# Kernel tuning notes

Measured on AMD Instinct MI355X. Metric: run time of the kernel, lower is better.

The kernel has to match this reference:

```python
import jax, jax.numpy as jnp
import numpy as np

KS = (7, 7)
ST = (3, 3)
PD = (3, 3)
DIM = 512
HID = 1960  # 40 * 49, divisible by kernel_shape


def _patch_flat_idx(out_h, out_w):
    kh, kw = KS; sh, sw = ST; ph, pw = PD
    oh = (out_h + 2 * ph - kh) // sh + 1
    ow = (out_w + 2 * pw - kw) // sw + 1
    Wp = out_w + 2 * pw
    iy = jnp.arange(kh)[:, None, None, None] + (jnp.arange(oh) * sh)[None, None, :, None]
    ix = jnp.arange(kw)[None, :, None, None] + (jnp.arange(ow) * sw)[None, None, None, :]
    # (kh, kw, oh, ow) flat index into padded image
    return (iy * Wp + ix), oh, ow


def fold(patches, out_h, out_w):
    # patches: (B, C*kh*kw, L) -> (B, C, out_h, out_w), overlap-add like F.fold
    kh, kw = KS; ph, pw = PD
    idx, oh, ow = _patch_flat_idx(out_h, out_w)
    B, CK, L = patches.shape
    C = CK // (kh * kw)
    Hp, Wp = out_h + 2 * ph, out_w + 2 * pw
    p = patches.reshape(B, C, kh, kw, oh, ow)
    out = jnp.zeros((B, C, Hp * Wp), patches.dtype)
    out = out.at[:, :, idx.reshape(-1)].add(p.reshape(B, C, -1))
    return out.reshape(B, C, Hp, Wp)[:, :, ph:ph + out_h, pw:pw + out_w]


def unfold(img, out_h, out_w):
    # img: (B, C, H, W) -> (B, C*kh*kw, L), like F.unfold
    kh, kw = KS; ph, pw = PD
    idx, oh, ow = _patch_flat_idx(out_h, out_w)
    B, C = img.shape[:2]
    imgp = jnp.pad(img, ((0, 0), (0, 0), (ph, ph), (pw, pw)))
    flat = imgp.reshape(B, C, -1)
    g = flat[:, :, idx.reshape(-1)].reshape(B, C, kh, kw, oh, ow)
    return g.reshape(B, C * kh * kw, oh * ow)


def setup_inputs() -> dict:
    key = jax.random.key(0)
    k1, k2, k3, k4, k5 = jax.random.split(key, 5)
    x = jax.random.normal(k1, (2, 5760, DIM), dtype=jnp.float32)
    W1 = jax.random.normal(k2, (HID, DIM), dtype=jnp.float32) * 0.02
    b1 = jax.random.normal(k3, (HID,), dtype=jnp.float32) * 0.02
    W2 = jax.random.normal(k4, (DIM, HID), dtype=jnp.float32) * 0.02
    b2 = jax.random.normal(k5, (DIM,), dtype=jnp.float32) * 0.02
    return {"x": x, "W1": W1, "b1": b1, "W2": W2, "b2": b2, "out_h": 60, "out_w": 108}


def reference(x, W1, b1, W2, b2, out_h, out_w):
    kh, kw = KS; sh, sw = ST; ph, pw = PD
    oh = (out_h + 2 * ph - kh) // sh + 1
    ow = (out_w + 2 * pw - kw) // sw + 1
    n_vecs = oh * ow
    h = jnp.einsum('bnd,hd->bnh', x, W1) + b1          # (b, n, HID)
    b_, n, c = h.shape
    p = h.reshape(-1, n_vecs, c).transpose(0, 2, 1)     # (B', c, L)
    folded = fold(p, out_h, out_w)                      # (B', c//49, H, W)
    ones = jnp.ones((p.shape[0], kh * kw, n_vecs), h.dtype)
    norm = fold(ones, out_h, out_w)                     # (B', 1, H, W)
    y = unfold(folded / norm, out_h, out_w)             # (B', c, L)
    y = y.transpose(0, 2, 1).reshape(b_, n, c)
    out = jnp.einsum('bnh,dh->bnd', jax.nn.gelu(y, approximate=False), W2) + b2
    return out
```

## Files before the change

### kernel.cpp

```cpp
#include <hip/hip_runtime.h>
#include <cmath>

#define M_ROWS   11520
#define DIM      512
#define HID      1960
#define HIDP     2048
#define KP2      1984
#define OH       20
#define OW       36
#define LVEC     720
#define NCH      40
#define BPRIME   16
#define HP       66
#define WP       114

typedef unsigned short u16;
typedef __bf16 bf16x8 __attribute__((ext_vector_type(8)));
typedef float  f32x4  __attribute__((ext_vector_type(4)));

__device__ __forceinline__ u16 f2bf(float f) {
    unsigned u = __float_as_uint(f);
    u += 0x7fffu + ((u >> 16) & 1u);
    return (u16)(u >> 16);
}
__device__ __forceinline__ float bf2f(u16 h) {
    return __uint_as_float(((unsigned)h) << 16);
}

__device__ __forceinline__ void gload_lds16(const void* g, void* l) {
    __builtin_amdgcn_global_load_lds(
        (const __attribute__((address_space(1))) void*)g,
        (__attribute__((address_space(3))) void*)l, 16, 0, 0);
}
__device__ __forceinline__ void gload_lds4(const void* g, void* l) {
    __builtin_amdgcn_global_load_lds(
        (const __attribute__((address_space(1))) void*)g,
        (__attribute__((address_space(3))) void*)l, 4, 0, 0);
}

#define CVT_XB   5760
#define CVT_W1B  1024
#define CVT_W2B  1024
#define CVT_Z    270
__global__ __launch_bounds__(256) void cvt_all(const float* __restrict__ x,
                                               const float* __restrict__ W1,
                                               const float* __restrict__ W2,
                                               u16* __restrict__ xb,
                                               u16* __restrict__ W1b,
                                               u16* __restrict__ W2b,
                                               u16* __restrict__ g2) {
    const int b = blockIdx.x;
    const int tid = threadIdx.x;
    ushort4 o;
    if (b < CVT_XB) {
        int i = (b * 256 + tid) * 4;
        float4 v = *(const float4*)(x + i);
        o.x = f2bf(v.x); o.y = f2bf(v.y); o.z = f2bf(v.z); o.w = f2bf(v.w);
        *(ushort4*)(xb + i) = o;
    } else if (b < CVT_XB + CVT_W1B) {
        int i = ((b - CVT_XB) * 256 + tid) * 4;
        if (i < HID * DIM) {
            float4 v = *(const float4*)(W1 + i);
            o.x = f2bf(v.x); o.y = f2bf(v.y); o.z = f2bf(v.z); o.w = f2bf(v.w);
        } else {
            o.x = o.y = o.z = o.w = 0;
        }
        *(ushort4*)(W1b + i) = o;
    } else if (b < CVT_XB + CVT_W1B + CVT_W2B) {
        int i = ((b - CVT_XB - CVT_W1B) * 256 + tid) * 4;
        int d = i / HIDP, c = i - d * HIDP;
        if (c < HID) {
            float4 v = *(const float4*)(W2 + (size_t)d * HID + c);
            o.x = f2bf(v.x); o.y = f2bf(v.y); o.z = f2bf(v.z); o.w = f2bf(v.w);
        } else {
            o.x = o.y = o.z = o.w = 0;
        }
        *(ushort4*)(W2b + i) = o;
    } else {
        int i = ((b - CVT_XB - CVT_W1B - CVT_W2B) * 256 + tid) * 4;
        int row = i / 24, c = i - row * 24;
        o.x = o.y = o.z = o.w = 0;
        *(ushort4*)(g2 + (size_t)row * HIDP + HID + c) = o;
    }
}

template <int OUT_BF16, int BN>
__global__ __launch_bounds__(512) void gemm_bt(const u16* __restrict__ A,
                                               const u16* __restrict__ B,
                                               const float* __restrict__ bias,
                                               int biasN, void* __restrict__ Cout,
                                               int N, int K, int ldk) {
    constexpr int WN = BN / 2;
    constexpr int NU = WN / 16;
    constexpr int BCH = BN * 8;

    __shared__ u16 sA[128 * 64];
    __shared__ u16 sB[BN * 64];

    const int tid  = threadIdx.x;
    const int ntn  = N / BN;
    const int NB   = gridDim.x;
    const int v    = (blockIdx.x & 7) * (NB >> 3) + (blockIdx.x >> 3);
    const int bm   = v / ntn;
    const int bn   = v - bm * ntn;
    const int lane = tid & 63;
    const int wv   = tid >> 6;
    const int wm   = (wv >> 1) * 32;
    const int wn   = (wv & 1) * WN;
    const int r    = lane & 15;
    const int quad = lane >> 4;

    const size_t Arow0 = (size_t)bm * 128 * ldk;
    const size_t Brow0 = (size_t)bn * BN * ldk;

    f32x4 acc[2][NU] = {};

    for (int kt = 0; kt < K; kt += 64) {
        __syncthreads();
#pragma unroll
        for (int i = 0; i < 2; i++) {
            int e   = i * 512 + tid;
            int row = e >> 3;
            int cp  = e & 7;
            int cg  = cp ^ (row & 7);
            gload_lds16(A + Arow0 + (size_t)row * ldk + kt + cg * 8, (char*)sA + e * 16);
        }
#pragma unroll
        for (int i = 0; i < BCH / 512; i++) {
            int e   = i * 512 + tid;
            int row = e >> 3;
            int cp  = e & 7;
            int cg  = cp ^ (row & 7);
            gload_lds16(B + Brow0 + (size_t)row * ldk + kt + cg * 8, (char*)sB + e * 16);
        }
        __syncthreads();
#pragma unroll
        for (int kk = 0; kk < 2; kk++) {
            bf16x8 af[2], bg[NU];
#pragma unroll
            for (int t = 0; t < 2; t++) {
                int row = wm + t * 16 + r;
                int c   = (kk * 4 + quad) ^ (row & 7);
                af[t] = *(const bf16x8*)(sA + row * 64 + c * 8);
            }
#pragma unroll
            for (int u = 0; u < NU; u++) {
                int row = wn + u * 16 + r;
                int c   = (kk * 4 + quad) ^ (row & 7);
                bg[u] = *(const bf16x8*)(sB + row * 64 + c * 8);
            }
#pragma unroll
            for (int t = 0; t < 2; t++)
#pragma unroll
                for (int u = 0; u < NU; u++)
                    acc[t][u] = __builtin_amdgcn_mfma_f32_16x16x32_bf16(
                        af[t], bg[u], acc[t][u], 0, 0, 0);
        }
    }

    const int gm0 = bm * 128 + wm;
    const int gn0 = bn * BN + wn;
#pragma unroll
    for (int u = 0; u < NU; u++) {
        int gn = gn0 + u * 16 + r;
        float bv = (gn < biasN) ? bias[gn] : 0.0f;
#pragma unroll
        for (int t = 0; t < 2; t++) {
            int gm = gm0 + t * 16 + quad * 4;
#pragma unroll
            for (int q = 0; q < 4; q++) {
                float v2 = acc[t][u][q] + bv;
                if (OUT_BF16)
                    ((u16*)Cout)[(size_t)(gm + q) * N + gn] = f2bf(v2);
                else
                    ((float*)Cout)[(size_t)(gm + q) * N + gn] = v2;
            }
        }
    }
}

__global__ __launch_bounds__(512) void mid_fused(const u16* __restrict__ hg,
                                                 u16* __restrict__ g2) {
    __shared__ u16 sh[12 * OW * 50];
    __shared__ u16 sG[34 * WP];
    __shared__ u16 rowoff[10 * OW];
    __shared__ u16 kidx[49];

    const int b  = blockIdx.x;
    const int bp = b / (NCH * 2);
    const int rr = b - bp * (NCH * 2);
    const int ch = rr >> 1;
    const int s  = rr & 1;
    const int o0 = s * 10;
    const int lo = s * 8;
    const int n0 = bp * LVEC;
    const int c0 = ch * 49;
    const int c0e = c0 & ~1;
    const int koff = c0 - c0e;
    const int tid = threadIdx.x;

    if (tid < 10 * OW) {
        int oy = tid / OW, ox = tid - oy * OW;
        rowoff[tid] = (u16)(342 * oy + 3 * ox);
    } else if (tid < 10 * OW + 49) {
        int k = tid - 10 * OW;
        int ky = k / 7;
        kidx[k] = (u16)(114 * ky + (k - 7 * ky));
    }

    {
        const char* hb = (const char*)(hg + (size_t)(n0 + lo * OW) * HIDP + c0e);
        for (int i = tid; i < 12 * OW * 25; i += 512) {
            int l = i / 25, j = i - l * 25;
            gload_lds4(hb + (size_t)l * (HIDP * 2) + j * 4, (char*)sh + i * 4);
        }
    }
    __syncthreads();

    const int px = tid & 127;
    const int rg = tid >> 7;
    if (px < WP) {
        const bool pxin = (px >= 3) && (px <= 110);
        const int kx0 = px % 3;
        int  ct[3];
        bool vx[3];
        int  cx = 0;
#pragma unroll
        for (int dx = 0; dx < 3; dx++) {
            int kx = kx0 + 3 * dx, rx = px - kx;
            bool ok = pxin && (kx <= 6) && (rx >= 0) && (rx <= 105);
            vx[dx] = ok;
            ct[dx] = ok ? ((rx / 3) * 50 + kx) : 0;
            cx += ok ? 1 : 0;
        }
        const float fcx = (cx == 3) ? (1.0f / 3.0f) : ((cx == 2) ? 0.5f : 1.0f);

        for (int pr = rg; pr < 34; pr += 4) {
            int py = 3 * o0 + pr;
            float val = 0.0f;
            if (pxin && py >= 3 && py <= 62) {
                int ky0 = py % 3;
                float sum = 0.0f;
                int cy = 0;
#pragma unroll
                for (int dy = 0; dy < 3; dy++) {
                    int ky = ky0 + 3 * dy, ry = py - ky;
                    if (ky <= 6 && ry >= 0 && ry <= 57) {
                        int rt = (ry / 3 - lo) * (OW * 50) + ky * 7 + koff;
                        cy++;
                        float v0 = bf2f(sh[rt + ct[0]]);
                        float v1 = bf2f(sh[rt + ct[1]]);
                        float v2 = bf2f(sh[rt + ct[2]]);
                        sum += vx[0] ? v0 : 0.0f;
                        sum += vx[1] ? v1 : 0.0f;
                        sum += vx[2] ? v2 : 0.0f;
                    }
                }
                float fcy = (cy == 3) ? (1.0f / 3.0f) : ((cy == 2) ? 0.5f : 1.0f);
                float m = sum * fcx * fcy;
                val = 0.5f * m * (1.0f + erff(m * 0.70710678118654752f));
            }
            sG[pr * WP + px] = f2bf(val);
        }
    }
    __syncthreads();

    {
        u16* g2row = g2 + (size_t)(n0 + o0 * OW) * HIDP + c0;
        int l = tid / 49;
        int k = tid - l * 49;
        int soff = l * HIDP + k;
        for (int i = tid; i < 10 * OW * 49; i += 512) {
            g2row[soff] = sG[rowoff[l] + kidx[k]];
            l += 10; k += 22; soff += 10 * HIDP + 22;
            if (k >= 49) { k -= 49; l += 1; soff += HIDP - 49; }
        }
    }
}

extern "C" void kernel_launch(void* const* d_in, const int* in_sizes, int n_in,
                              void* d_out, int out_size, void* d_ws, size_t ws_size,
                              hipStream_t stream) {
    (void)in_sizes; (void)n_in; (void)out_size; (void)ws_size;
    const float* x  = (const float*)d_in[0];
    const float* W1 = (const float*)d_in[1];
    const float* b1 = (const float*)d_in[2];
    const float* W2 = (const float*)d_in[3];
    const float* b2 = (const float*)d_in[4];
    float* out = (float*)d_out;

    char* ws = (char*)d_ws;
    u16* xb  = (u16*)(ws);
    u16* W1b = (u16*)(ws + 11796480);
    u16* W2b = (u16*)(ws + 13893632);
    u16* hg  = (u16*)(ws + 15990784);
    u16* g2  = (u16*)(ws + 63176704);

    cvt_all<<<CVT_XB + CVT_W1B + CVT_W2B + CVT_Z, 256, 0, stream>>>(
        x, W1, W2, xb, W1b, W2b, g2);

    gemm_bt<1, 128><<<(M_ROWS / 128) * (HIDP / 128), 512, 0, stream>>>(
        xb, W1b, b1, HID, (void*)hg, HIDP, DIM, DIM);

    mid_fused<<<BPRIME * NCH * 2, 512, 0, stream>>>(hg, g2);

    gemm_bt<0, 64><<<(M_ROWS / 128) * (DIM / 64), 512, 0, stream>>>(
        g2, W2b, b2, DIM, (void*)out, DIM, KP2, HIDP);
}
```

Baseline: 188.3 us.

## Split mid_fused tiles horizontally and load patches with 16-byte LDS transfers

The fold/normalize/gelu/unfold kernel now splits each tile into two horizontal halves, doubling the grid to 2560 blocks with a smaller shared-memory footprint. The patch load switches from 4-byte to 16-byte global-to-LDS transfers on 8-element-aligned channel windows, with index math done by multiply-shift division. The aim is better occupancy and fewer, wider memory transactions, at the cost of halo columns loaded twice and extra index arithmetic in the write-back loop.

```diff
diff --git a/kernel.cpp b/kernel.cpp
--- a/kernel.cpp
+++ b/kernel.cpp
@@ -31,11 +31,6 @@
     __builtin_amdgcn_global_load_lds(
         (const __attribute__((address_space(1))) void*)g,
         (__attribute__((address_space(3))) void*)l, 16, 0, 0);
-}
-__device__ __forceinline__ void gload_lds4(const void* g, void* l) {
-    __builtin_amdgcn_global_load_lds(
-        (const __attribute__((address_space(1))) void*)g,
-        (__attribute__((address_space(3))) void*)l, 4, 0, 0);
 }
 
 #define CVT_XB   5760
@@ -181,61 +176,57 @@
 
 __global__ __launch_bounds__(512) void mid_fused(const u16* __restrict__ hg,
                                                  u16* __restrict__ g2) {
-    __shared__ u16 sh[12 * OW * 50];
-    __shared__ u16 sG[34 * WP];
-    __shared__ u16 rowoff[10 * OW];
-    __shared__ u16 kidx[49];
-
-    const int b  = blockIdx.x;
-    const int bp = b / (NCH * 2);
-    const int rr = b - bp * (NCH * 2);
-    const int ch = rr >> 1;
-    const int s  = rr & 1;
-    const int o0 = s * 10;
-    const int lo = s * 8;
-    const int n0 = bp * LVEC;
-    const int c0 = ch * 49;
-    const int c0e = c0 & ~1;
-    const int koff = c0 - c0e;
+    __shared__ u16 sh[12 * 20 * 56];
+    __shared__ u16 sG[34 * 58];
+
+    const int b   = blockIdx.x;
+    const int bp  = b / (NCH * 4);
+    const int rr  = b - bp * (NCH * 4);
+    const int ch  = rr >> 2;
+    const int s   = (rr >> 1) & 1;
+    const int xh  = rr & 1;
+    const int o0  = s * 10;
+    const int lo  = s * 8;
+    const int ox0 = xh * 16;
+    const int n0  = bp * LVEC;
+    const int c0  = ch * 49;
+    const int c0f = c0 & ~7;
+    const int koff = c0 & 7;
     const int tid = threadIdx.x;
 
-    if (tid < 10 * OW) {
-        int oy = tid / OW, ox = tid - oy * OW;
-        rowoff[tid] = (u16)(342 * oy + 3 * ox);
-    } else if (tid < 10 * OW + 49) {
-        int k = tid - 10 * OW;
-        int ky = k / 7;
-        kidx[k] = (u16)(114 * ky + (k - 7 * ky));
-    }
-
     {
-        const char* hb = (const char*)(hg + (size_t)(n0 + lo * OW) * HIDP + c0e);
-        for (int i = tid; i < 12 * OW * 25; i += 512) {
-            int l = i / 25, j = i - l * 25;
-            gload_lds4(hb + (size_t)l * (HIDP * 2) + j * 4, (char*)sh + i * 4);
+        const char* hb = (const char*)(hg + (size_t)(n0 + lo * 36 + ox0) * HIDP + c0f);
+        for (int t = tid; t < 12 * 20 * 7; t += 512) {
+            int r   = (int)(((unsigned)t * 74899u) >> 19);
+            int c   = t - r * 7;
+            int loy = (int)(((unsigned)r * 3277u) >> 16);
+            int oxl = r - 20 * loy;
+            gload_lds16(hb + (size_t)(loy * 36 + oxl) * (HIDP * 2) + c * 16,
+                        (char*)sh + t * 16);
         }
     }
     __syncthreads();
 
-    const int px = tid & 127;
-    const int rg = tid >> 7;
-    if (px < WP) {
-        const bool pxin = (px >= 3) && (px <= 110);
-        const int kx0 = px % 3;
+    const int pxl = tid & 63;
+    const int rg  = tid >> 6;
+    if (pxl < 58) {
+        const int  pxg  = pxl + 54 * xh;
+        const bool pxin = (pxg >= 3) && (pxg <= 110);
+        const int  kx0  = pxg % 3;
         int  ct[3];
         bool vx[3];
         int  cx = 0;
 #pragma unroll
         for (int dx = 0; dx < 3; dx++) {
-            int kx = kx0 + 3 * dx, rx = px - kx;
+            int kx = kx0 + 3 * dx, rx = pxg - kx;
             bool ok = pxin && (kx <= 6) && (rx >= 0) && (rx <= 105);
             vx[dx] = ok;
-            ct[dx] = ok ? ((rx / 3) * 50 + kx) : 0;
+            ct[dx] = ok ? ((rx / 3) - ox0) * 56 + kx : 0;
             cx += ok ? 1 : 0;
         }
         const float fcx = (cx == 3) ? (1.0f / 3.0f) : ((cx == 2) ? 0.5f : 1.0f);
 
-        for (int pr = rg; pr < 34; pr += 4) {
+        for (int pr = rg; pr < 34; pr += 8) {
             int py = 3 * o0 + pr;
             float val = 0.0f;
             if (pxin && py >= 3 && py <= 62) {
@@ -246,7 +237,7 @@
                 for (int dy = 0; dy < 3; dy++) {
                     int ky = ky0 + 3 * dy, ry = py - ky;
                     if (ky <= 6 && ry >= 0 && ry <= 57) {
-                        int rt = (ry / 3 - lo) * (OW * 50) + ky * 7 + koff;
+                        int rt = (ry / 3 - lo) * (20 * 56) + ky * 7 + koff;
                         cy++;
                         float v0 = bf2f(sh[rt + ct[0]]);
                         float v1 = bf2f(sh[rt + ct[1]]);
@@ -260,20 +251,22 @@
                 float m = sum * fcx * fcy;
                 val = 0.5f * m * (1.0f + erff(m * 0.70710678118654752f));
             }
-            sG[pr * WP + px] = f2bf(val);
+            sG[pr * 58 + pxl] = f2bf(val);
         }
     }
     __syncthreads();
 
     {
-        u16* g2row = g2 + (size_t)(n0 + o0 * OW) * HIDP + c0;
-        int l = tid / 49;
-        int k = tid - l * 49;
-        int soff = l * HIDP + k;
-        for (int i = tid; i < 10 * OW * 49; i += 512) {
-            g2row[soff] = sG[rowoff[l] + kidx[k]];
-            l += 10; k += 22; soff += 10 * HIDP + 22;
-            if (k >= 49) { k -= 49; l += 1; soff += HIDP - 49; }
+        u16* g2row = g2 + (size_t)(n0 + o0 * 36 + 18 * xh) * HIDP + c0;
+        for (int j = tid; j < 10 * 18 * 49; j += 512) {
+            int l2 = (int)(((unsigned)j * 42800u) >> 21);
+            int k  = j - l2 * 49;
+            int oy = (int)(((unsigned)l2 * 57u) >> 10);
+            int ox = l2 - 18 * oy;
+            int ky = (int)(((unsigned)k * 37u) >> 8);
+            int kx = k - 7 * ky;
+            g2row[(size_t)(oy * 36 + ox) * HIDP + k] =
+                sG[(3 * oy + ky) * 58 + 3 * ox + kx];
         }
     }
 }
@@ -302,7 +295,7 @@
     gemm_bt<1, 128><<<(M_ROWS / 128) * (HIDP / 128), 512, 0, stream>>>(
         xb, W1b, b1, HID, (void*)hg, HIDP, DIM, DIM);
 
-    mid_fused<<<BPRIME * NCH * 2, 512, 0, stream>>>(hg, g2);
+    mid_fused<<<BPRIME * NCH * 4, 512, 0, stream>>>(hg, g2);
 
     gemm_bt<0, 64><<<(M_ROWS / 128) * (DIM / 64), 512, 0, stream>>>(
         g2, W2b, b2, DIM, (void*)out, DIM, KP2, HIDP);
```

Result: no change. 186.8 us (-0.8%).
